# Optimization experiments

Measured on AMD Instinct MI355X. Metric: run time of the kernel, lower is better.

Reference implementation:

```python
import jax, jax.numpy as jnp
import numpy as np

D_MODEL = 1024
OUTPUT_DIM = 1024
NUM_HEADS = 16
HEAD_DIM = D_MODEL // NUM_HEADS


def _xavier(key, shape):
    fan_in, fan_out = shape[1], shape[0]
    limit = float(np.sqrt(6.0 / (fan_in + fan_out)))
    return jax.random.uniform(key, shape, jnp.float32, -limit, limit)


def setup_inputs() -> dict:
    key = jax.random.key(0)
    k_h, k_q, k_k, k_o = jax.random.split(key, 4)
    H = jax.random.normal(k_h, (2, 2048, D_MODEL), dtype=jnp.float32)
    # nn.Linear weights are [out, in]; xavier_uniform on weights, default (uniform) biases left as zeros-equivalent
    Wq = _xavier(k_q, (D_MODEL, D_MODEL))
    bq = jnp.zeros((D_MODEL,), jnp.float32)
    Wk = _xavier(k_k, (D_MODEL, D_MODEL))
    bk = jnp.zeros((D_MODEL,), jnp.float32)
    Wo = _xavier(k_o, (OUTPUT_DIM, D_MODEL))
    bo = jnp.zeros((OUTPUT_DIM,), jnp.float32)
    return {"H": H, "Wq": Wq, "bq": bq, "Wk": Wk, "bk": bk, "Wo": Wo, "bo": bo}


def reference(H, Wq, bq, Wk, bk, Wo, bo):
    B, S, _ = H.shape
    Q = H @ Wq.T + bq  # [B,S,D]
    K = H @ Wk.T + bk
    # split heads -> [B,nh,S,hd]
    Qh = Q.reshape(B, S, NUM_HEADS, HEAD_DIM).transpose(0, 2, 1, 3)
    Kh = K.reshape(B, S, NUM_HEADS, HEAD_DIM).transpose(0, 2, 1, 3)
    Vh = H.reshape(B, S, NUM_HEADS, HEAD_DIM).transpose(0, 2, 1, 3)
    scale = 1.0 / jnp.sqrt(jnp.float32(HEAD_DIM))
    A = jnp.einsum('bhqd,bhkd->bhqk', Qh, Kh) * scale  # [B,nh,S,S]
    A = jax.nn.softmax(A, axis=-1)
    out = jnp.einsum('bhqk,bhkd->bhqd', A, Vh)  # [B,nh,S,hd]
    out = out.transpose(0, 2, 1, 3).reshape(B, S, D_MODEL)
    return out @ Wo.T + bo
```

## Files before the change

### kernel.cpp

```cpp
#include <hip/hip_runtime.h>
#include <stdint.h>

#define BB 2
#define SS 2048
#define DD 1024
#define NH 16
#define HD 64
#define MM 4096

typedef __bf16 bf16x8 __attribute__((ext_vector_type(8)));
typedef __bf16 bf16x4 __attribute__((ext_vector_type(4)));
typedef float  f32x4  __attribute__((ext_vector_type(4)));

__device__ __forceinline__ unsigned short f2bf(float f) {
    __bf16 h = (__bf16)f;
    return __builtin_bit_cast(unsigned short, h);
}

__device__ __forceinline__ void async_cp16(const void* g, const void* l) {
    __builtin_amdgcn_global_load_lds(
        (const __attribute__((address_space(1))) void*)(uintptr_t)g,
        (__attribute__((address_space(3))) void*)(uint32_t)(uintptr_t)l,
        16, 0, 0);
}

__device__ __forceinline__ f32x4 mfma16(bf16x8 a, bf16x8 b, f32x4 c) {
    return __builtin_amdgcn_mfma_f32_16x16x32_bf16(a, b, c, 0, 0, 0);
}

__global__ __launch_bounds__(256) void k_prep(const float* __restrict__ H,
                                              const float* __restrict__ Wq,
                                              const float* __restrict__ Wk,
                                              const float* __restrict__ Wo,
                                              unsigned short* __restrict__ Hb,
                                              unsigned short* __restrict__ Vt,
                                              unsigned short* __restrict__ Wqb,
                                              unsigned short* __restrict__ Wkb,
                                              unsigned short* __restrict__ Wob) {
    __shared__ float tile[128][68];
    const int bx = blockIdx.x;
    const int t = threadIdx.x;
    if (bx >= 512) {
        int g = bx - 512;
        const float* src; unsigned short* dst; int base;
        if (g < 512)       { src = Wq; dst = Wqb; base = g; }
        else if (g < 1024) { src = Wk; dst = Wkb; base = g - 512; }
        else               { src = Wo; dst = Wob; base = g - 1024; }
        int i = (base * 256 + t) * 8;
        float4 a = *(const float4*)(src + i);
        float4 b = *(const float4*)(src + i + 4);
        unsigned short o[8];
        o[0] = f2bf(a.x); o[1] = f2bf(a.y); o[2] = f2bf(a.z); o[3] = f2bf(a.w);
        o[4] = f2bf(b.x); o[5] = f2bf(b.y); o[6] = f2bf(b.z); o[7] = f2bf(b.w);
        *(ulonglong2*)(dst + i) = *(ulonglong2*)o;
        return;
    }
    const int sb = bx & 15, h = (bx >> 4) & 15, b = bx >> 8;
    const int col4 = t & 15;
    const int srow0 = t >> 4;
#pragma unroll
    for (int p = 0; p < 8; ++p) {
        int s = p * 16 + srow0;
        float4 v = *(const float4*)(H + (size_t)(b * SS + sb * 128 + s) * DD + h * HD + col4 * 4);
        *(float4*)&tile[s][col4 * 4] = v;
    }
    __syncthreads();
#pragma unroll
    for (int it = 0; it < 4; ++it) {
        int task = it * 256 + t;
        int s = task >> 3;
        int dg = task & 7;
        unsigned short pk[8];
#pragma unroll
        for (int j = 0; j < 8; ++j) pk[j] = f2bf(tile[s][dg * 8 + j]);
        *(ulonglong2*)(Hb + (size_t)(b * SS + sb * 128 + s) * DD + h * HD + dg * 8) = *(ulonglong2*)pk;
    }
#pragma unroll
    for (int it = 0; it < 4; ++it) {
        int task = it * 256 + t;
        int d = task >> 4;
        int sg = task & 15;
        unsigned short pk[8];
#pragma unroll
        for (int j = 0; j < 8; ++j) pk[j] = f2bf(tile[sg * 8 + j][d]);
        *(ulonglong2*)(Vt + (size_t)((b * NH + h) * HD + d) * SS + sb * 128 + sg * 8) = *(ulonglong2*)pk;
    }
}

template <int TM, bool BF16OUT>
__device__ __forceinline__ void gemm_body(const unsigned short* __restrict__ A,
                                          const unsigned short* __restrict__ Bt,
                                          const float* __restrict__ bias,
                                          void* __restrict__ Cp, float oscale,
                                          int mBase, int nBase) {
    constexpr int MT = TM / 32;
    constexpr int AR = TM / 32;
    __shared__ unsigned short lsA[2][TM * 64];
    __shared__ unsigned short lsB[2][128 * 64];
    const int tid = threadIdx.x;
    const int lane = tid & 63;
    const int w = tid >> 6;
    const int wm = w & 1, wn = w >> 1;
    const int r = lane & 15, quad = lane >> 4;

    const unsigned short* gA[AR]; uint laOff[AR];
#pragma unroll
    for (int t = 0; t < AR; ++t) {
        int l = t * 256 + tid;
        int c = l ^ ((l >> 3) & 7);
        int row = c >> 3, kc = c & 7;
        gA[t] = A + (size_t)(mBase + row) * 1024 + kc * 8;
        laOff[t] = l * 8;
    }
    const unsigned short* gB[4]; uint lbOff[4];
#pragma unroll
    for (int t = 0; t < 4; ++t) {
        int l = t * 256 + tid;
        int c = l ^ ((l >> 3) & 7);
        int row = c >> 3, kc = c & 7;
        gB[t] = Bt + (size_t)(nBase + row) * 1024 + kc * 8;
        lbOff[t] = l * 8;
    }
    uint aOff[2][MT], bOff[2][4];
#pragma unroll
    for (int hh = 0; hh < 2; ++hh) {
#pragma unroll
        for (int mt = 0; mt < MT; ++mt) {
            int rowA = wm * (TM / 2) + mt * 16 + r;
            int c = rowA * 8 + hh * 4 + quad;
            aOff[hh][mt] = (uint)((c ^ ((c >> 3) & 7)) * 8);
        }
#pragma unroll
        for (int nt = 0; nt < 4; ++nt) {
            int rowB = wn * 64 + nt * 16 + r;
            int c = rowB * 8 + hh * 4 + quad;
            bOff[hh][nt] = (uint)((c ^ ((c >> 3) & 7)) * 8);
        }
    }

    f32x4 acc[MT][4];
#pragma unroll
    for (int i = 0; i < MT; ++i)
#pragma unroll
        for (int j = 0; j < 4; ++j) acc[i][j] = f32x4{0.f, 0.f, 0.f, 0.f};

    auto stage = [&](int buf) {
#pragma unroll
        for (int t = 0; t < AR; ++t) { async_cp16(gA[t], &lsA[buf][laOff[t]]); gA[t] += 64; }
#pragma unroll
        for (int t = 0; t < 4; ++t)  { async_cp16(gB[t], &lsB[buf][lbOff[t]]); gB[t] += 64; }
    };

    stage(0);
    for (int kb = 0; kb < 16; ++kb) {
        const int cur = kb & 1;
        __syncthreads();
        if (kb + 1 < 16) stage(cur ^ 1);

#pragma unroll
        for (int hh = 0; hh < 2; ++hh) {
            bf16x8 af[MT], bf[4];
#pragma unroll
            for (int mt = 0; mt < MT; ++mt) af[mt] = *(const bf16x8*)&lsA[cur][aOff[hh][mt]];
#pragma unroll
            for (int nt = 0; nt < 4; ++nt)  bf[nt] = *(const bf16x8*)&lsB[cur][bOff[hh][nt]];
#pragma unroll
            for (int mt = 0; mt < MT; ++mt)
#pragma unroll
                for (int nt = 0; nt < 4; ++nt)
                    acc[mt][nt] = mfma16(af[mt], bf[nt], acc[mt][nt]);
        }
    }

    float bv[4];
#pragma unroll
    for (int nt = 0; nt < 4; ++nt) bv[nt] = bias[nBase + wn * 64 + nt * 16 + r];
#pragma unroll
    for (int mt = 0; mt < MT; ++mt)
#pragma unroll
        for (int nt = 0; nt < 4; ++nt) {
            int colg = nBase + wn * 64 + nt * 16 + r;
#pragma unroll
            for (int reg = 0; reg < 4; ++reg) {
                int rowg = mBase + wm * (TM / 2) + mt * 16 + quad * 4 + reg;
                float v = (acc[mt][nt][reg] + bv[nt]) * oscale;
                if (BF16OUT)
                    ((unsigned short*)Cp)[(size_t)rowg * 1024 + colg] = f2bf(v);
                else
                    ((float*)Cp)[(size_t)rowg * 1024 + colg] = v;
            }
        }
}

#define QSCALE 0.1803368801111137f

__global__ __launch_bounds__(256) void k_gemm_qk(const unsigned short* __restrict__ Hb,
                                                 const unsigned short* __restrict__ Wqb,
                                                 const unsigned short* __restrict__ Wkb,
                                                 const float* __restrict__ bq,
                                                 const float* __restrict__ bk,
                                                 unsigned short* __restrict__ Q,
                                                 unsigned short* __restrict__ K) {
    const int id = blockIdx.x;
    const int x = id >> 6, yp = id & 63;
    const int z = yp >> 5, y = yp & 31;
    const unsigned short* Bt = z ? Wkb : Wqb;
    const float* bias = z ? bk : bq;
    unsigned short* C = z ? K : Q;
    float os = z ? 1.0f : QSCALE;
    gemm_body<128, true>(Hb, Bt, bias, C, os, y * 128, x * 128);
}

__global__ __launch_bounds__(256) void k_gemm_out(const unsigned short* __restrict__ Ctx,
                                                  const unsigned short* __restrict__ Wob,
                                                  const float* __restrict__ bo,
                                                  float* __restrict__ Out) {
    const int id = blockIdx.x;
    const int x = id >> 6, y = id & 63;
    gemm_body<64, false>(Ctx, Wob, bo, Out, 1.0f, y * 64, x * 128);
}

__global__ __launch_bounds__(256) void k_attn(const unsigned short* __restrict__ Q,
                                              const unsigned short* __restrict__ K,
                                              const unsigned short* __restrict__ Vt,
                                              unsigned short* __restrict__ Ctx) {
    __shared__ unsigned short lsK[2][128 * 64];
    __shared__ unsigned short lsV[2][128 * 64];
    __shared__ unsigned short lsP[4 * 2048];
    const int tid = threadIdx.x;
    const int lane = tid & 63;
    const int w = tid >> 6;
    const int r = lane & 15, quad = lane >> 4;
    const int id = blockIdx.x;
    const int xcd = id & 7, j = id >> 3;
    const int hb = xcd + 8 * (j & 3);
    const int qb = j >> 2;
    const int h = hb & 15, b = hb >> 4;

    bf16x8 aq[2][2];
#pragma unroll
    for (int sub = 0; sub < 2; ++sub) {
        const int qrow = qb * 128 + w * 32 + sub * 16 + r;
        const size_t qoff = (size_t)(b * SS + qrow) * DD + h * HD;
        aq[sub][0] = *(const bf16x8*)(Q + qoff + quad * 8);
        aq[sub][1] = *(const bf16x8*)(Q + qoff + 32 + quad * 8);
    }

    f32x4 accO[2][4];
#pragma unroll
    for (int sub = 0; sub < 2; ++sub)
#pragma unroll
        for (int nt = 0; nt < 4; ++nt) accO[sub][nt] = f32x4{0.f, 0.f, 0.f, 0.f};
    float lsum[2][4] = {{0.f, 0.f, 0.f, 0.f}, {0.f, 0.f, 0.f, 0.f}};

    const unsigned short* gK[4]; const unsigned short* gV[4]; uint lO[4];
#pragma unroll
    for (int t = 0; t < 4; ++t) {
        int l = t * 256 + tid;
        int c = l ^ ((l >> 3) & 7);
        int half = c >> 9, kc = c & 7;
        int rr = (c >> 3) & 63;
        int srow = half * 64 + 4 * (rr & 15) + (rr >> 4);
        gK[t] = K + (size_t)(b * SS + srow) * DD + h * HD + kc * 8;
        gV[t] = Vt + (size_t)((b * NH + h) * HD + rr) * SS + half * 64 + kc * 8;
        lO[t] = l * 8;
    }
    uint off[2][4];
#pragma unroll
    for (int t = 0; t < 2; ++t)
#pragma unroll
        for (int nt = 0; nt < 4; ++nt) {
            int rowX = nt * 16 + r;
            int c = rowX * 8 + t * 4 + quad;
            off[t][nt] = (uint)((c ^ ((c >> 3) & 7)) * 8);
        }
    uint pw[4], pr[2];
#pragma unroll
    for (int reg = 0; reg < 4; ++reg) {
        int prow = quad * 4 + reg;
        pw[reg] = (uint)(prow * 64 + ((r >> 1) ^ (prow & 7)) * 8 + (r & 1) * 4);
    }
#pragma unroll
    for (int t = 0; t < 2; ++t)
        pr[t] = (uint)(r * 64 + ((4 * t + quad) ^ (r & 7)) * 8);
    unsigned short* Pw = lsP + w * 2048;

    auto stage = [&](int buf) {
#pragma unroll
        for (int t = 0; t < 4; ++t) {
            async_cp16(gK[t], &lsK[buf][lO[t]]); gK[t] += 128 * DD;
            async_cp16(gV[t], &lsV[buf][lO[t]]); gV[t] += 128;
        }
    };

    stage(0);
    for (int kt = 0; kt < 16; ++kt) {
        const int cur = kt & 1;
        __syncthreads();
        if (kt + 1 < 16) stage(cur ^ 1);

#pragma unroll
        for (int half = 0; half < 2; ++half) {
            const uint ho = (uint)half * 4096;

            f32x4 s[2][4];
#pragma unroll
            for (int sub = 0; sub < 2; ++sub)
#pragma unroll
                for (int nt = 0; nt < 4; ++nt) s[sub][nt] = f32x4{0.f, 0.f, 0.f, 0.f};
#pragma unroll
            for (int t = 0; t < 2; ++t)
#pragma unroll
                for (int nt = 0; nt < 4; ++nt) {
                    bf16x8 bk = *(const bf16x8*)&lsK[cur][ho + off[t][nt]];
                    s[0][nt] = mfma16(aq[0][t], bk, s[0][nt]);
                    s[1][nt] = mfma16(aq[1][t], bk, s[1][nt]);
                }

#pragma unroll
            for (int sub = 0; sub < 2; ++sub)
#pragma unroll
                for (int reg = 0; reg < 4; ++reg) {
                    float p0 = __builtin_amdgcn_exp2f(s[sub][0][reg]);
                    float p1 = __builtin_amdgcn_exp2f(s[sub][1][reg]);
                    float p2 = __builtin_amdgcn_exp2f(s[sub][2][reg]);
                    float p3 = __builtin_amdgcn_exp2f(s[sub][3][reg]);
                    lsum[sub][reg] += (p0 + p1) + (p2 + p3);
                    bf16x4 pk = {(__bf16)p0, (__bf16)p1, (__bf16)p2, (__bf16)p3};
                    *(bf16x4*)&Pw[sub * 1024 + pw[reg]] = pk;
                }

#pragma unroll
            for (int t = 0; t < 2; ++t) {
                bf16x8 ap0 = *(const bf16x8*)&Pw[pr[t]];
                bf16x8 ap1 = *(const bf16x8*)&Pw[1024 + pr[t]];
#pragma unroll
                for (int nt = 0; nt < 4; ++nt) {
                    bf16x8 bv = *(const bf16x8*)&lsV[cur][ho + off[t][nt]];
                    accO[0][nt] = mfma16(ap0, bv, accO[0][nt]);
                    accO[1][nt] = mfma16(ap1, bv, accO[1][nt]);
                }
            }
        }
    }

#pragma unroll
    for (int sub = 0; sub < 2; ++sub) {
        float linv[4];
#pragma unroll
        for (int reg = 0; reg < 4; ++reg) {
            float l = lsum[sub][reg];
            l += __shfl_xor(l, 1);
            l += __shfl_xor(l, 2);
            l += __shfl_xor(l, 4);
            l += __shfl_xor(l, 8);
            linv[reg] = 1.0f / l;
        }
#pragma unroll
        for (int nt = 0; nt < 4; ++nt) {
            int d = nt * 16 + r;
#pragma unroll
            for (int reg = 0; reg < 4; ++reg) {
                int qr = qb * 128 + w * 32 + sub * 16 + quad * 4 + reg;
                Ctx[(size_t)(b * SS + qr) * DD + h * HD + d] = f2bf(accO[sub][nt][reg] * linv[reg]);
            }
        }
    }
}

extern "C" void kernel_launch(void* const* d_in, const int* in_sizes, int n_in,
                              void* d_out, int out_size, void* d_ws, size_t ws_size,
                              hipStream_t stream) {
    (void)in_sizes; (void)n_in; (void)out_size; (void)ws_size;
    const float* H  = (const float*)d_in[0];
    const float* Wq = (const float*)d_in[1];
    const float* bq = (const float*)d_in[2];
    const float* Wk = (const float*)d_in[3];
    const float* bk = (const float*)d_in[4];
    const float* Wo = (const float*)d_in[5];
    const float* bo = (const float*)d_in[6];
    float* Out = (float*)d_out;

    char* ws = (char*)d_ws;
    unsigned short* Hb  = (unsigned short*)(ws);
    unsigned short* Qb  = (unsigned short*)(ws + 8388608);
    unsigned short* Kb  = (unsigned short*)(ws + 16777216);
    unsigned short* Ctx = (unsigned short*)(ws + 25165824);
    unsigned short* Vt  = (unsigned short*)(ws + 33554432);
    unsigned short* Wqb = (unsigned short*)(ws + 41943040);
    unsigned short* Wkb = (unsigned short*)(ws + 44040192);
    unsigned short* Wob = (unsigned short*)(ws + 46137344);

    k_prep<<<dim3(2048), dim3(256), 0, stream>>>(H, Wq, Wk, Wo, Hb, Vt, Wqb, Wkb, Wob);
    k_gemm_qk<<<dim3(512), dim3(256), 0, stream>>>(Hb, Wqb, Wkb, bq, bk, Qb, Kb);
    k_attn<<<dim3(512), dim3(256), 0, stream>>>(Qb, Kb, Vt, Ctx);
    k_gemm_out<<<dim3(512), dim3(256), 0, stream>>>(Ctx, Wob, bo, Out);
}
```

Measured before the change: 167.7 us.

## Retile GEMMs to 8-wave 128x128 blocks with 32-wide K steps

The shared GEMM body now runs with 512 threads (8 waves), each wave computing a 64x32 sub-tile. The K step is halved to 32, so each thread issues a single async 16-byte copy for A and one for B per stage. The output projection switches from 64x128 tiles on 512 blocks to 128x128 tiles on 256 blocks. The aim is more waves per tile to hide latency and more operand reuse in the output GEMM, at the cost of twice as many barriers per K loop and less MFMA work between them.

```diff
diff --git a/kernel.cpp b/kernel.cpp
--- a/kernel.cpp
+++ b/kernel.cpp
@@ -87,102 +87,83 @@
     }
 }
 
-template <int TM, bool BF16OUT>
+template <bool BF16OUT>
 __device__ __forceinline__ void gemm_body(const unsigned short* __restrict__ A,
                                           const unsigned short* __restrict__ Bt,
                                           const float* __restrict__ bias,
                                           void* __restrict__ Cp, float oscale,
                                           int mBase, int nBase) {
-    constexpr int MT = TM / 32;
-    constexpr int AR = TM / 32;
-    __shared__ unsigned short lsA[2][TM * 64];
-    __shared__ unsigned short lsB[2][128 * 64];
+    __shared__ unsigned short lsA[2][128 * 32];
+    __shared__ unsigned short lsB[2][128 * 32];
     const int tid = threadIdx.x;
     const int lane = tid & 63;
     const int w = tid >> 6;
     const int wm = w & 1, wn = w >> 1;
     const int r = lane & 15, quad = lane >> 4;
 
-    const unsigned short* gA[AR]; uint laOff[AR];
-#pragma unroll
-    for (int t = 0; t < AR; ++t) {
-        int l = t * 256 + tid;
-        int c = l ^ ((l >> 3) & 7);
-        int row = c >> 3, kc = c & 7;
-        gA[t] = A + (size_t)(mBase + row) * 1024 + kc * 8;
-        laOff[t] = l * 8;
-    }
-    const unsigned short* gB[4]; uint lbOff[4];
-#pragma unroll
-    for (int t = 0; t < 4; ++t) {
-        int l = t * 256 + tid;
-        int c = l ^ ((l >> 3) & 7);
-        int row = c >> 3, kc = c & 7;
-        gB[t] = Bt + (size_t)(nBase + row) * 1024 + kc * 8;
-        lbOff[t] = l * 8;
-    }
-    uint aOff[2][MT], bOff[2][4];
-#pragma unroll
-    for (int hh = 0; hh < 2; ++hh) {
-#pragma unroll
-        for (int mt = 0; mt < MT; ++mt) {
-            int rowA = wm * (TM / 2) + mt * 16 + r;
-            int c = rowA * 8 + hh * 4 + quad;
-            aOff[hh][mt] = (uint)((c ^ ((c >> 3) & 7)) * 8);
-        }
-#pragma unroll
-        for (int nt = 0; nt < 4; ++nt) {
-            int rowB = wn * 64 + nt * 16 + r;
-            int c = rowB * 8 + hh * 4 + quad;
-            bOff[hh][nt] = (uint)((c ^ ((c >> 3) & 7)) * 8);
-        }
-    }
-
-    f32x4 acc[MT][4];
-#pragma unroll
-    for (int i = 0; i < MT; ++i)
-#pragma unroll
-        for (int j = 0; j < 4; ++j) acc[i][j] = f32x4{0.f, 0.f, 0.f, 0.f};
+    {
+    }
+    int l0 = tid;
+    int c0 = l0 ^ ((l0 >> 3) & 7);
+    int row0 = c0 >> 2, kc0 = c0 & 3;
+    const unsigned short* gA = A + (size_t)(mBase + row0) * 1024 + kc0 * 8;
+    const unsigned short* gB = Bt + (size_t)(nBase + row0) * 1024 + kc0 * 8;
+    const uint lOff = (uint)l0 * 8;
+
+    uint aOff[4], bOff[2];
+#pragma unroll
+    for (int mt = 0; mt < 4; ++mt) {
+        int rowA = wm * 64 + mt * 16 + r;
+        int c = rowA * 4 + quad;
+        aOff[mt] = (uint)((c ^ ((c >> 3) & 7)) * 8);
+    }
+#pragma unroll
+    for (int nt = 0; nt < 2; ++nt) {
+        int rowB = wn * 32 + nt * 16 + r;
+        int c = rowB * 4 + quad;
+        bOff[nt] = (uint)((c ^ ((c >> 3) & 7)) * 8);
+    }
+
+    f32x4 acc[4][2];
+#pragma unroll
+    for (int i = 0; i < 4; ++i)
+#pragma unroll
+        for (int j = 0; j < 2; ++j) acc[i][j] = f32x4{0.f, 0.f, 0.f, 0.f};
 
     auto stage = [&](int buf) {
-#pragma unroll
-        for (int t = 0; t < AR; ++t) { async_cp16(gA[t], &lsA[buf][laOff[t]]); gA[t] += 64; }
-#pragma unroll
-        for (int t = 0; t < 4; ++t)  { async_cp16(gB[t], &lsB[buf][lbOff[t]]); gB[t] += 64; }
+        async_cp16(gA, &lsA[buf][lOff]); gA += 32;
+        async_cp16(gB, &lsB[buf][lOff]); gB += 32;
     };
 
     stage(0);
-    for (int kb = 0; kb < 16; ++kb) {
+    for (int kb = 0; kb < 32; ++kb) {
         const int cur = kb & 1;
         __syncthreads();
-        if (kb + 1 < 16) stage(cur ^ 1);
-
-#pragma unroll
-        for (int hh = 0; hh < 2; ++hh) {
-            bf16x8 af[MT], bf[4];
-#pragma unroll
-            for (int mt = 0; mt < MT; ++mt) af[mt] = *(const bf16x8*)&lsA[cur][aOff[hh][mt]];
-#pragma unroll
-            for (int nt = 0; nt < 4; ++nt)  bf[nt] = *(const bf16x8*)&lsB[cur][bOff[hh][nt]];
-#pragma unroll
-            for (int mt = 0; mt < MT; ++mt)
-#pragma unroll
-                for (int nt = 0; nt < 4; ++nt)
-                    acc[mt][nt] = mfma16(af[mt], bf[nt], acc[mt][nt]);
-        }
-    }
-
-    float bv[4];
-#pragma unroll
-    for (int nt = 0; nt < 4; ++nt) bv[nt] = bias[nBase + wn * 64 + nt * 16 + r];
-#pragma unroll
-    for (int mt = 0; mt < MT; ++mt)
-#pragma unroll
-        for (int nt = 0; nt < 4; ++nt) {
-            int colg = nBase + wn * 64 + nt * 16 + r;
+        if (kb + 1 < 32) stage(cur ^ 1);
+
+        bf16x8 af[4], bf[2];
+#pragma unroll
+        for (int mt = 0; mt < 4; ++mt) af[mt] = *(const bf16x8*)&lsA[cur][aOff[mt]];
+#pragma unroll
+        for (int nt = 0; nt < 2; ++nt) bf[nt] = *(const bf16x8*)&lsB[cur][bOff[nt]];
+#pragma unroll
+        for (int mt = 0; mt < 4; ++mt)
+#pragma unroll
+            for (int nt = 0; nt < 2; ++nt)
+                acc[mt][nt] = mfma16(af[mt], bf[nt], acc[mt][nt]);
+    }
+
+    float bv[2];
+#pragma unroll
+    for (int nt = 0; nt < 2; ++nt) bv[nt] = bias[nBase + wn * 32 + nt * 16 + r];
+#pragma unroll
+    for (int mt = 0; mt < 4; ++mt)
+#pragma unroll
+        for (int nt = 0; nt < 2; ++nt) {
+            int colg = nBase + wn * 32 + nt * 16 + r;
 #pragma unroll
             for (int reg = 0; reg < 4; ++reg) {
-                int rowg = mBase + wm * (TM / 2) + mt * 16 + quad * 4 + reg;
+                int rowg = mBase + wm * 64 + mt * 16 + quad * 4 + reg;
                 float v = (acc[mt][nt][reg] + bv[nt]) * oscale;
                 if (BF16OUT)
                     ((unsigned short*)Cp)[(size_t)rowg * 1024 + colg] = f2bf(v);
@@ -194,7 +175,7 @@
 
 #define QSCALE 0.1803368801111137f
 
-__global__ __launch_bounds__(256) void k_gemm_qk(const unsigned short* __restrict__ Hb,
+__global__ __launch_bounds__(512) void k_gemm_qk(const unsigned short* __restrict__ Hb,
                                                  const unsigned short* __restrict__ Wqb,
                                                  const unsigned short* __restrict__ Wkb,
                                                  const float* __restrict__ bq,
@@ -208,16 +189,16 @@
     const float* bias = z ? bk : bq;
     unsigned short* C = z ? K : Q;
     float os = z ? 1.0f : QSCALE;
-    gemm_body<128, true>(Hb, Bt, bias, C, os, y * 128, x * 128);
-}
-
-__global__ __launch_bounds__(256) void k_gemm_out(const unsigned short* __restrict__ Ctx,
+    gemm_body<true>(Hb, Bt, bias, C, os, y * 128, x * 128);
+}
+
+__global__ __launch_bounds__(512) void k_gemm_out(const unsigned short* __restrict__ Ctx,
                                                   const unsigned short* __restrict__ Wob,
                                                   const float* __restrict__ bo,
                                                   float* __restrict__ Out) {
     const int id = blockIdx.x;
-    const int x = id >> 6, y = id & 63;
-    gemm_body<64, false>(Ctx, Wob, bo, Out, 1.0f, y * 64, x * 128);
+    const int x = id >> 5, y = id & 31;
+    gemm_body<false>(Ctx, Wob, bo, Out, 1.0f, y * 128, x * 128);
 }
 
 __global__ __launch_bounds__(256) void k_attn(const unsigned short* __restrict__ Q,
@@ -392,7 +373,7 @@
     unsigned short* Wob = (unsigned short*)(ws + 46137344);
 
     k_prep<<<dim3(2048), dim3(256), 0, stream>>>(H, Wq, Wk, Wo, Hb, Vt, Wqb, Wkb, Wob);
-    k_gemm_qk<<<dim3(512), dim3(256), 0, stream>>>(Hb, Wqb, Wkb, bq, bk, Qb, Kb);
+    k_gemm_qk<<<dim3(512), dim3(512), 0, stream>>>(Hb, Wqb, Wkb, bq, bk, Qb, Kb);
     k_attn<<<dim3(512), dim3(256), 0, stream>>>(Qb, Kb, Vt, Ctx);
-    k_gemm_out<<<dim3(512), dim3(256), 0, stream>>>(Ctx, Wob, bo, Out);
-}
+    k_gemm_out<<<dim3(256), dim3(512), 0, stream>>>(Ctx, Wob, bo, Out);
+}
```

Result: slower. 173.4 us (+3.4%).

## Split attention across two key halves and merge partial outputs in a separate kernel

Applied to the files above, without the earlier changes.

Each attention block now processes only half of the key sequence, doubling the grid to 1024 blocks and halving the K/V shared-memory tiles. Unnormalized partial outputs and row sums are written to workspace, and a new merge kernel sums the two halves and normalizes. The aim is more concurrent blocks per CU and better latency hiding. The cost is extra global traffic for the partials and an additional kernel launch.

```diff
diff --git a/kernel.cpp b/kernel.cpp
--- a/kernel.cpp
+++ b/kernel.cpp
@@ -223,9 +223,11 @@
 __global__ __launch_bounds__(256) void k_attn(const unsigned short* __restrict__ Q,
                                               const unsigned short* __restrict__ K,
                                               const unsigned short* __restrict__ Vt,
-                                              unsigned short* __restrict__ Ctx) {
-    __shared__ unsigned short lsK[2][128 * 64];
-    __shared__ unsigned short lsV[2][128 * 64];
+                                              unsigned short* __restrict__ Od0,
+                                              unsigned short* __restrict__ Od1,
+                                              float* __restrict__ Ld) {
+    __shared__ unsigned short lsK[2][64 * 64];
+    __shared__ unsigned short lsV[2][64 * 64];
     __shared__ unsigned short lsP[4 * 2048];
     const int tid = threadIdx.x;
     const int lane = tid & 63;
@@ -234,8 +236,10 @@
     const int id = blockIdx.x;
     const int xcd = id & 7, j = id >> 3;
     const int hb = xcd + 8 * (j & 3);
-    const int qb = j >> 2;
+    const int rem = j >> 2;
+    const int qb = rem & 15, kh = rem >> 4;
     const int h = hb & 15, b = hb >> 4;
+    const int kbase = kh * 1024;
 
     bf16x8 aq[2][2];
 #pragma unroll
@@ -253,16 +257,15 @@
         for (int nt = 0; nt < 4; ++nt) accO[sub][nt] = f32x4{0.f, 0.f, 0.f, 0.f};
     float lsum[2][4] = {{0.f, 0.f, 0.f, 0.f}, {0.f, 0.f, 0.f, 0.f}};
 
-    const unsigned short* gK[4]; const unsigned short* gV[4]; uint lO[4];
-#pragma unroll
-    for (int t = 0; t < 4; ++t) {
+    const unsigned short* gK[2]; const unsigned short* gV[2]; uint lO[2];
+#pragma unroll
+    for (int t = 0; t < 2; ++t) {
         int l = t * 256 + tid;
         int c = l ^ ((l >> 3) & 7);
-        int half = c >> 9, kc = c & 7;
-        int rr = (c >> 3) & 63;
-        int srow = half * 64 + 4 * (rr & 15) + (rr >> 4);
-        gK[t] = K + (size_t)(b * SS + srow) * DD + h * HD + kc * 8;
-        gV[t] = Vt + (size_t)((b * NH + h) * HD + rr) * SS + half * 64 + kc * 8;
+        int row = c >> 3, kc = c & 7;
+        int srow = 4 * (row & 15) + (row >> 4);
+        gK[t] = K + (size_t)(b * SS + kbase + srow) * DD + h * HD + kc * 8;
+        gV[t] = Vt + (size_t)((b * NH + h) * HD + row) * SS + kbase + kc * 8;
         lO[t] = l * 8;
     }
     uint off[2][4];
@@ -287,9 +290,9 @@
 
     auto stage = [&](int buf) {
 #pragma unroll
-        for (int t = 0; t < 4; ++t) {
-            async_cp16(gK[t], &lsK[buf][lO[t]]); gK[t] += 128 * DD;
-            async_cp16(gV[t], &lsV[buf][lO[t]]); gV[t] += 128;
+        for (int t = 0; t < 2; ++t) {
+            async_cp16(gK[t], &lsK[buf][lO[t]]); gK[t] += 64 * DD;
+            async_cp16(gV[t], &lsV[buf][lO[t]]); gV[t] += 64;
         }
     };
 
@@ -299,54 +302,50 @@
         __syncthreads();
         if (kt + 1 < 16) stage(cur ^ 1);
 
-#pragma unroll
-        for (int half = 0; half < 2; ++half) {
-            const uint ho = (uint)half * 4096;
-
-            f32x4 s[2][4];
-#pragma unroll
-            for (int sub = 0; sub < 2; ++sub)
-#pragma unroll
-                for (int nt = 0; nt < 4; ++nt) s[sub][nt] = f32x4{0.f, 0.f, 0.f, 0.f};
-#pragma unroll
-            for (int t = 0; t < 2; ++t)
-#pragma unroll
-                for (int nt = 0; nt < 4; ++nt) {
-                    bf16x8 bk = *(const bf16x8*)&lsK[cur][ho + off[t][nt]];
-                    s[0][nt] = mfma16(aq[0][t], bk, s[0][nt]);
-                    s[1][nt] = mfma16(aq[1][t], bk, s[1][nt]);
-                }
-
-#pragma unroll
-            for (int sub = 0; sub < 2; ++sub)
-#pragma unroll
-                for (int reg = 0; reg < 4; ++reg) {
-                    float p0 = __builtin_amdgcn_exp2f(s[sub][0][reg]);
-                    float p1 = __builtin_amdgcn_exp2f(s[sub][1][reg]);
-                    float p2 = __builtin_amdgcn_exp2f(s[sub][2][reg]);
-                    float p3 = __builtin_amdgcn_exp2f(s[sub][3][reg]);
-                    lsum[sub][reg] += (p0 + p1) + (p2 + p3);
-                    bf16x4 pk = {(__bf16)p0, (__bf16)p1, (__bf16)p2, (__bf16)p3};
-                    *(bf16x4*)&Pw[sub * 1024 + pw[reg]] = pk;
-                }
-
-#pragma unroll
-            for (int t = 0; t < 2; ++t) {
-                bf16x8 ap0 = *(const bf16x8*)&Pw[pr[t]];
-                bf16x8 ap1 = *(const bf16x8*)&Pw[1024 + pr[t]];
-#pragma unroll
-                for (int nt = 0; nt < 4; ++nt) {
-                    bf16x8 bv = *(const bf16x8*)&lsV[cur][ho + off[t][nt]];
-                    accO[0][nt] = mfma16(ap0, bv, accO[0][nt]);
-                    accO[1][nt] = mfma16(ap1, bv, accO[1][nt]);
-                }
-            }
-        }
-    }
-
+        f32x4 s[2][4];
+#pragma unroll
+        for (int sub = 0; sub < 2; ++sub)
+#pragma unroll
+            for (int nt = 0; nt < 4; ++nt) s[sub][nt] = f32x4{0.f, 0.f, 0.f, 0.f};
+#pragma unroll
+        for (int t = 0; t < 2; ++t)
+#pragma unroll
+            for (int nt = 0; nt < 4; ++nt) {
+                bf16x8 bk = *(const bf16x8*)&lsK[cur][off[t][nt]];
+                s[0][nt] = mfma16(aq[0][t], bk, s[0][nt]);
+                s[1][nt] = mfma16(aq[1][t], bk, s[1][nt]);
+            }
+
+#pragma unroll
+        for (int sub = 0; sub < 2; ++sub)
+#pragma unroll
+            for (int reg = 0; reg < 4; ++reg) {
+                float p0 = __builtin_amdgcn_exp2f(s[sub][0][reg]);
+                float p1 = __builtin_amdgcn_exp2f(s[sub][1][reg]);
+                float p2 = __builtin_amdgcn_exp2f(s[sub][2][reg]);
+                float p3 = __builtin_amdgcn_exp2f(s[sub][3][reg]);
+                lsum[sub][reg] += (p0 + p1) + (p2 + p3);
+                bf16x4 pk = {(__bf16)p0, (__bf16)p1, (__bf16)p2, (__bf16)p3};
+                *(bf16x4*)&Pw[sub * 1024 + pw[reg]] = pk;
+            }
+
+#pragma unroll
+        for (int t = 0; t < 2; ++t) {
+            bf16x8 ap0 = *(const bf16x8*)&Pw[pr[t]];
+            bf16x8 ap1 = *(const bf16x8*)&Pw[1024 + pr[t]];
+#pragma unroll
+            for (int nt = 0; nt < 4; ++nt) {
+                bf16x8 bv = *(const bf16x8*)&lsV[cur][off[t][nt]];
+                accO[0][nt] = mfma16(ap0, bv, accO[0][nt]);
+                accO[1][nt] = mfma16(ap1, bv, accO[1][nt]);
+            }
+        }
+    }
+
+    unsigned short* Od = kh ? Od1 : Od0;
 #pragma unroll
     for (int sub = 0; sub < 2; ++sub) {
-        float linv[4];
+        float lred[4];
 #pragma unroll
         for (int reg = 0; reg < 4; ++reg) {
             float l = lsum[sub][reg];
@@ -354,7 +353,7 @@
             l += __shfl_xor(l, 2);
             l += __shfl_xor(l, 4);
             l += __shfl_xor(l, 8);
-            linv[reg] = 1.0f / l;
+            lred[reg] = l;
         }
 #pragma unroll
         for (int nt = 0; nt < 4; ++nt) {
@@ -362,10 +361,36 @@
 #pragma unroll
             for (int reg = 0; reg < 4; ++reg) {
                 int qr = qb * 128 + w * 32 + sub * 16 + quad * 4 + reg;
-                Ctx[(size_t)(b * SS + qr) * DD + h * HD + d] = f2bf(accO[sub][nt][reg] * linv[reg]);
-            }
-        }
-    }
+                Od[(size_t)(b * SS + qr) * DD + h * HD + d] = f2bf(accO[sub][nt][reg]);
+            }
+        }
+        if (r == 0) {
+#pragma unroll
+            for (int reg = 0; reg < 4; ++reg) {
+                int qr = qb * 128 + w * 32 + sub * 16 + quad * 4 + reg;
+                Ld[((size_t)(kh * BB + b) * NH + h) * SS + qr] = lred[reg];
+            }
+        }
+    }
+}
+
+__global__ __launch_bounds__(256) void k_merge(const unsigned short* __restrict__ O0,
+                                               const unsigned short* __restrict__ O1,
+                                               const float* __restrict__ Ld,
+                                               unsigned short* __restrict__ Ctx) {
+    int i = (blockIdx.x * 256 + threadIdx.x) * 8;
+    int row = i >> 10, c = i & 1023;
+    int b = row >> 11, q = row & 2047, h = c >> 6;
+    float l0 = Ld[((size_t)(b)*NH + h) * SS + q];
+    float l1 = Ld[((size_t)(BB + b) * NH + h) * SS + q];
+    float rinv = 1.0f / (l0 + l1);
+    bf16x8 a = *(const bf16x8*)(O0 + i);
+    bf16x8 bb = *(const bf16x8*)(O1 + i);
+    unsigned short o[8];
+#pragma unroll
+    for (int j = 0; j < 8; ++j)
+        o[j] = f2bf(((float)a[j] + (float)bb[j]) * rinv);
+    *(ulonglong2*)(Ctx + i) = *(ulonglong2*)o;
 }
 
 extern "C" void kernel_launch(void* const* d_in, const int* in_sizes, int n_in,
@@ -390,9 +415,13 @@
     unsigned short* Wqb = (unsigned short*)(ws + 41943040);
     unsigned short* Wkb = (unsigned short*)(ws + 44040192);
     unsigned short* Wob = (unsigned short*)(ws + 46137344);
+    unsigned short* Od0 = Hb;
+    unsigned short* Od1 = (unsigned short*)(ws + 48234496);
+    float*          Ld  = (float*)(ws + 56623104);
 
     k_prep<<<dim3(2048), dim3(256), 0, stream>>>(H, Wq, Wk, Wo, Hb, Vt, Wqb, Wkb, Wob);
     k_gemm_qk<<<dim3(512), dim3(256), 0, stream>>>(Hb, Wqb, Wkb, bq, bk, Qb, Kb);
-    k_attn<<<dim3(512), dim3(256), 0, stream>>>(Qb, Kb, Vt, Ctx);
+    k_attn<<<dim3(1024), dim3(256), 0, stream>>>(Qb, Kb, Vt, Od0, Od1, Ld);
+    k_merge<<<dim3(2048), dim3(256), 0, stream>>>(Od0, Od1, Ld, Ctx);
     k_gemm_out<<<dim3(512), dim3(256), 0, stream>>>(Ctx, Wob, bo, Out);
 }
```

New measurement: 185.7 us. 10.8% more time.
